# Performance work log

Hardware: AMD Instinct MI355X
Metric: run time of the kernel (lower is better)

The kernel has to match this reference:

```python
import jax, jax.numpy as jnp
import numpy as np

N = 50000          # nodes
E = 1_600_000      # edges (avg degree 32, radius graph capped at 64 nbrs)
F_X = 32           # node feature dim
F_E = 8            # edge attr dim
RADIUS = 8.0       # radius used to normalize pair distance
EPS = 1e-5         # LayerNorm eps (torch default)


def _glorot(key, shape):
    fan_in = shape[0]
    return (jax.random.normal(key, shape, dtype=jnp.float32) / np.sqrt(fan_in)).astype(jnp.float32)


def setup_inputs() -> dict:
    key = jax.random.key(0)
    ks = jax.random.split(key, 16)
    x = jax.random.normal(ks[0], (N, F_X), dtype=jnp.float32)
    pos = jax.random.normal(ks[1], (N, 3), dtype=jnp.float32) * 10.0
    normal = jax.random.normal(ks[2], (N, 3), dtype=jnp.float32)
    normal = normal / jnp.linalg.norm(normal, axis=1, keepdims=True)
    edge_attr = jax.random.normal(ks[3], (E, F_E), dtype=jnp.float32)
    edge_index = jax.random.randint(ks[4], (2, E), 0, N, dtype=jnp.int64)
    d_in = F_X + 7 + F_E  # 47
    return {
        "x": x, "pos": pos, "normal": normal, "edge_attr": edge_attr,
        "edge_index": edge_index,
        # local MLP: [47 -> 64 -> 128], each block Linear->ReLU->LayerNorm
        "W1": _glorot(ks[5], (d_in, 64)), "b1": jnp.zeros((64,), jnp.float32),
        "g1": jnp.ones((64,), jnp.float32), "be1": jnp.zeros((64,), jnp.float32),
        "W2": _glorot(ks[6], (64, 128)), "b2": jnp.zeros((128,), jnp.float32),
        "g2": jnp.ones((128,), jnp.float32), "be2": jnp.zeros((128,), jnp.float32),
        # global MLP: [128 -> 256]
        "Wg": _glorot(ks[7], (128, 256)), "bg": jnp.zeros((256,), jnp.float32),
        "gg": jnp.ones((256,), jnp.float32), "beg": jnp.zeros((256,), jnp.float32),
    }


def _layernorm(h, g, b):
    mu = jnp.mean(h, axis=-1, keepdims=True)
    var = jnp.mean(jnp.square(h - mu), axis=-1, keepdims=True)
    return (h - mu) * jax.lax.rsqrt(var + EPS) * g + b


def _mlp_block(h, W, b, g, be):
    # Linear -> ReLU -> LayerNorm (Dropout inactive in eval mode)
    return _layernorm(jax.nn.relu(h @ W + b), g, be)


def _angle(v1, v2):
    cross = jnp.cross(v1, v2)
    return jnp.arctan2(jnp.linalg.norm(cross, axis=1), jnp.sum(v1 * v2, axis=1))


def reference(x, pos, normal, edge_attr, edge_index,
              W1, b1, g1, be1, W2, b2, g2, be2, Wg, bg, gg, beg):
    src = edge_index[0]  # j (source)
    dst = edge_index[1]  # i (target)
    pos_i, pos_j = pos[dst], pos[src]
    n_i, n_j = normal[dst], normal[src]
    pseudo = pos_j - pos_i                       # [E,3]
    a1 = _angle(n_i, pseudo)
    a2 = _angle(n_j, pseudo)
    a3 = _angle(n_i, n_j)
    ppf = jnp.stack([
        jnp.linalg.norm(pseudo, axis=1) / RADIUS,
        jnp.sin(a1), jnp.cos(a1),
        jnp.sin(a2), jnp.cos(a2),
        jnp.sin(a3), jnp.cos(a3),
    ], axis=1)                                   # [E,7]
    msg = jnp.concatenate([x[src], ppf, edge_attr], axis=1)  # [E,47]
    msg = _mlp_block(msg, W1, b1, g1, be1)       # [E,64]
    msg = _mlp_block(msg, W2, b2, g2, be2)       # [E,128]
    agg = jax.ops.segment_max(msg, dst, num_segments=N)      # [N,128]
    agg = jnp.where(jnp.isfinite(agg), agg, 0.0)  # nodes with no in-edges -> 0
    out = _mlp_block(agg, Wg, bg, gg, beg)       # [N,256]
    return out
```

## Files before the change

### kernel.cpp

```cpp
#include <hip/hip_runtime.h>
#include <hip/hip_bf16.h>
#include <math.h>


#define LN_EPS 1e-5f
#define EPB 128
#define SM 72
#define SP 130
#define AS 132

typedef __attribute__((ext_vector_type(8))) short bf16x8;
typedef __attribute__((ext_vector_type(4))) float floatx4;
typedef __attribute__((ext_vector_type(4))) short s4v;

__device__ __forceinline__ unsigned ord(float f) {
    int i = __float_as_int(f);
    return (i >= 0) ? ((unsigned)i | 0x80000000u) : ~((unsigned)i);
}
__device__ __forceinline__ float unord(unsigned u) {
    int i = (u & 0x80000000u) ? (int)(u & 0x7fffffffu) : ~(int)u;
    return __int_as_float(i);
}
__device__ __forceinline__ unsigned short f2b(float f) {
    unsigned u = __float_as_uint(f);
    return (unsigned short)((u + 0x7FFFu + ((u >> 16) & 1u)) >> 16);
}
__device__ __forceinline__ float b2f(unsigned short h) {
    return __uint_as_float((unsigned)h << 16);
}

__global__ void hist_kernel(const int* __restrict__ ei, unsigned* __restrict__ deg, int E) {
    int e = blockIdx.x * 256 + threadIdx.x;
    if (e < E) atomicAdd(&deg[ei[E + e]], 1u);
}

__global__ void scan1(const unsigned* __restrict__ deg, unsigned* __restrict__ part, int N) {
    __shared__ unsigned s[256];
    int i = blockIdx.x * 256 + threadIdx.x;
    s[threadIdx.x] = (i < N) ? deg[i] : 0u;
    __syncthreads();
    for (int st = 128; st > 0; st >>= 1) {
        if (threadIdx.x < st) s[threadIdx.x] += s[threadIdx.x + st];
        __syncthreads();
    }
    if (threadIdx.x == 0) part[blockIdx.x] = s[0];
}

__global__ void scan2(unsigned* __restrict__ part, int nb) {
    __shared__ unsigned s[256];
    int t = threadIdx.x;
    unsigned v = (t < nb) ? part[t] : 0u;
    s[t] = v;
    __syncthreads();
    for (int st = 1; st < 256; st <<= 1) {
        unsigned add = (t >= st) ? s[t - st] : 0u;
        __syncthreads();
        s[t] += add;
        __syncthreads();
    }
    if (t < nb) part[t] = s[t] - v;
}

__global__ void scan3(const unsigned* __restrict__ deg, const unsigned* __restrict__ part,
                      unsigned* __restrict__ off, int N) {
    __shared__ unsigned s[256];
    int i = blockIdx.x * 256 + threadIdx.x, t = threadIdx.x;
    unsigned v = (i < N) ? deg[i] : 0u;
    s[t] = v;
    __syncthreads();
    for (int st = 1; st < 256; st <<= 1) {
        unsigned add = (t >= st) ? s[t - st] : 0u;
        __syncthreads();
        s[t] += add;
        __syncthreads();
    }
    if (i < N) off[i] = part[blockIdx.x] + s[t] - v;
}

__global__ void scatter_kernel(const int* __restrict__ ei, unsigned* __restrict__ cursor,
                               unsigned* __restrict__ perm, int* __restrict__ dsts, int E) {
    int e = blockIdx.x * 256 + threadIdx.x;
    if (e >= E) return;
    int d = ei[E + e];
    unsigned pos = atomicAdd(&cursor[d], 1u);
    perm[pos] = (unsigned)e;
    dsts[pos] = d;
}

__global__ void wprep_kernel(const float* __restrict__ W1, const float* __restrict__ W2,
                             const float* __restrict__ Wg,
                             unsigned short* __restrict__ W1p, unsigned short* __restrict__ W2p,
                             unsigned short* __restrict__ Wgp)
{
    int t = threadIdx.x;
    for (int fl = t; fl < 8 * 64; fl += 256) {
        int fi = fl >> 6, l = fl & 63;
        int s = fi >> 2, nt = fi & 3;
        int n = nt * 16 + (l & 15);
        int kb = s * 32 + ((l >> 4) << 3);
        #pragma unroll
        for (int j = 0; j < 8; ++j) {
            int k = kb + j;
            W1p[fl * 8 + j] = f2b((k < 47) ? W1[k * 64 + n] : 0.f);
        }
    }
    for (int fl = t; fl < 16 * 64; fl += 256) {
        int fi = fl >> 6, l = fl & 63;
        int s = fi >> 3, nt = fi & 7;
        int n = nt * 16 + (l & 15);
        int kb = s * 32 + ((l >> 4) << 3);
        #pragma unroll
        for (int j = 0; j < 8; ++j)
            W2p[fl * 8 + j] = f2b(W2[(kb + j) * 128 + n]);
    }
    for (int fl = t; fl < 64 * 64; fl += 256) {
        int fi = fl >> 6, l = fl & 63;
        int s = fi >> 4, nt = fi & 15;
        int n = nt * 16 + (l & 15);
        int kb = s * 32 + ((l >> 4) << 3);
        #pragma unroll
        for (int j = 0; j < 8; ++j)
            Wgp[fl * 8 + j] = f2b(Wg[(size_t)(kb + j) * 256 + n]);
    }
}

__global__ __launch_bounds__(256, 2)
void edge_kernel(const float* __restrict__ x,
                 const float* __restrict__ pos,
                 const float* __restrict__ nrm,
                 const float* __restrict__ ea,
                 const int* __restrict__ ei,
                 const unsigned* __restrict__ perm,
                 const int* __restrict__ dsts,
                 const unsigned short* __restrict__ W1p, const float* __restrict__ b1,
                 const float* __restrict__ g1, const float* __restrict__ be1,
                 const unsigned short* __restrict__ W2p, const float* __restrict__ b2,
                 const float* __restrict__ g2, const float* __restrict__ be2,
                 unsigned* __restrict__ agg, int E)
{
    __shared__ unsigned short hbuf[EPB * SM];
    __shared__ unsigned short st[128 * SP];
    __shared__ int dloc[EPB];
    __shared__ short rstart[EPB], rend[EPB];
    __shared__ unsigned long long wmask[2];
    __shared__ int dprev_s, dnext_s;

    const int tid  = threadIdx.x;
    const int lane = tid & 63;
    const int half = tid >> 7;
    const int el   = tid & 127;
    const int base = blockIdx.x * EPB;
    const int p    = base + el;
    const bool valid = p < E;
    const int nvalid = (E - base < EPB) ? (E - base) : EPB;

    int dst = 0, src = 0, e = 0;
    if (valid) {
        e   = (int)perm[p];
        dst = dsts[p];
        src = ei[e];
    }
    if (half == 0) dloc[el] = valid ? dst : -1;
    if (tid == 0) {
        dprev_s = (blockIdx.x == 0) ? -1 : dsts[(size_t)base - 1];
        dnext_s = (base + EPB < E) ? dsts[base + EPB] : -1;
    }

    if (valid) {
        unsigned short* row = &hbuf[el * SM];
        if (half == 0) {
            const float4* xp = (const float4*)(x + (size_t)src * 32);
            #pragma unroll
            for (int q = 0; q < 4; ++q) {
                float4 v = xp[q];
                s4v h = { (short)f2b(v.x), (short)f2b(v.y), (short)f2b(v.z), (short)f2b(v.w) };
                *(s4v*)&row[4 * q] = h;
            }
            float pix = pos[3*dst+0], piy = pos[3*dst+1], piz = pos[3*dst+2];
            float pjx = pos[3*src+0], pjy = pos[3*src+1], pjz = pos[3*src+2];
            float dx = pjx - pix, dy = pjy - piy, dz = pjz - piz;
            float nix = nrm[3*dst+0], niy = nrm[3*dst+1], niz = nrm[3*dst+2];
            float njx = nrm[3*src+0], njy = nrm[3*src+1], njz = nrm[3*src+2];
            row[32] = f2b(sqrtf(dx*dx + dy*dy + dz*dz) * 0.125f);
            float cx, cy, cz, c2, d, den, inv, sn, cs;
            cx = niy*dz - niz*dy; cy = niz*dx - nix*dz; cz = nix*dy - niy*dx;
            c2 = cx*cx + cy*cy + cz*cz;  d = nix*dx + niy*dy + niz*dz;
            den = c2 + d*d;
            if (den > 0.f) { inv = rsqrtf(den); sn = sqrtf(c2)*inv; cs = d*inv; }
            else           { sn = 0.f; cs = 1.f; }
            row[33] = f2b(sn); row[34] = f2b(cs);
            cx = njy*dz - njz*dy; cy = njz*dx - njx*dz; cz = njx*dy - njy*dx;
            c2 = cx*cx + cy*cy + cz*cz;  d = njx*dx + njy*dy + njz*dz;
            den = c2 + d*d;
            if (den > 0.f) { inv = rsqrtf(den); sn = sqrtf(c2)*inv; cs = d*inv; }
            else           { sn = 0.f; cs = 1.f; }
            row[35] = f2b(sn); row[36] = f2b(cs);
            cx = niy*njz - niz*njy; cy = niz*njx - nix*njz; cz = nix*njy - niy*njx;
            c2 = cx*cx + cy*cy + cz*cz;  d = nix*njx + niy*njy + niz*njz;
            den = c2 + d*d;
            if (den > 0.f) { inv = rsqrtf(den); sn = sqrtf(c2)*inv; cs = d*inv; }
            else           { sn = 0.f; cs = 1.f; }
            row[37] = f2b(sn); row[38] = f2b(cs);
        } else {
            const float4* xp = (const float4*)(x + (size_t)src * 32) + 4;
            #pragma unroll
            for (int q = 0; q < 4; ++q) {
                float4 v = xp[q];
                s4v h = { (short)f2b(v.x), (short)f2b(v.y), (short)f2b(v.z), (short)f2b(v.w) };
                *(s4v*)&row[16 + 4 * q] = h;
            }
            const float4* ep = (const float4*)(ea + (size_t)e * 8);
            float4 a0 = ep[0], a1 = ep[1];
            row[39] = f2b(a0.x); row[40] = f2b(a0.y);
            row[41] = f2b(a0.z); row[42] = f2b(a0.w);
            row[43] = f2b(a1.x); row[44] = f2b(a1.y);
            row[45] = f2b(a1.z); row[46] = f2b(a1.w);
            row[47] = 0;
            s4v z = {0, 0, 0, 0};
            *(s4v*)&row[48] = z; *(s4v*)&row[52] = z;
            *(s4v*)&row[56] = z; *(s4v*)&row[60] = z;
        }
    }
    __syncthreads();

    bool is_start = false, is_end = false;
    if (tid < 128) {
        int dt = dloc[tid];
        bool isv = tid < nvalid;
        is_start = isv && (tid == 0 || dloc[tid - 1] != dt);
        is_end   = isv && (tid == nvalid - 1 || dloc[tid + 1] != dt);
    }
    {
        unsigned long long mb = __ballot(is_start);
        if ((tid >> 6) < 2 && lane == 0) wmask[tid >> 6] = mb;
    }
    __syncthreads();
    int nr;
    {
        unsigned long long m0 = wmask[0], m1 = wmask[1];
        nr = __popcll(m0) + __popcll(m1);
        if (tid < 128) {
            int widr = tid >> 6;
            int rid = (widr ? __popcll(m0) : 0)
                    + __popcll((widr ? m1 : m0) & ((1ull << lane) - 1ull));
            if (is_start) rstart[rid] = (short)tid;
            if (is_end)   rend[is_start ? rid : rid - 1] = (short)tid;
        }
    }

    const int wid  = __builtin_amdgcn_readfirstlane(tid >> 6);
    const int quad = lane >> 4, col = lane & 15;
    const int mb0  = wid * 32;

    {
        bf16x8 w1f[8];
        const bf16x8* W1v = (const bf16x8*)W1p;
        #pragma unroll
        for (int i = 0; i < 8; ++i) w1f[i] = W1v[i * 64 + lane];
        float b1v[4], g1v[4], e1v[4];
        #pragma unroll
        for (int nt = 0; nt < 4; ++nt) {
            b1v[nt] = b1[nt*16 + col]; g1v[nt] = g1[nt*16 + col]; e1v[nt] = be1[nt*16 + col];
        }
        #pragma unroll
        for (int t = 0; t < 2; ++t) {
            const int mb = mb0 + t * 16;
            floatx4 acc[4] = {{0,0,0,0},{0,0,0,0},{0,0,0,0},{0,0,0,0}};
            #pragma unroll
            for (int s = 0; s < 2; ++s) {
                const unsigned short* ap = &hbuf[(mb + col) * SM + s*32 + quad*8];
                union { s4v h[2]; bf16x8 v; } u;
                u.h[0] = *(const s4v*)ap; u.h[1] = *(const s4v*)(ap + 4);
                #pragma unroll
                for (int nt = 0; nt < 4; ++nt)
                    acc[nt] = __builtin_amdgcn_mfma_f32_16x16x32_bf16(u.v, w1f[s*4+nt], acc[nt], 0, 0, 0);
            }
            float ps[4] = {0,0,0,0}, p2[4] = {0,0,0,0};
            #pragma unroll
            for (int nt = 0; nt < 4; ++nt)
                #pragma unroll
                for (int r = 0; r < 4; ++r) {
                    float v = fmaxf(acc[nt][r] + b1v[nt], 0.f);
                    acc[nt][r] = v; ps[r] += v; p2[r] += v * v;
                }
            #pragma unroll
            for (int r = 0; r < 4; ++r) {
                #pragma unroll
                for (int m = 1; m < 16; m <<= 1) {
                    ps[r] += __shfl_xor(ps[r], m);
                    p2[r] += __shfl_xor(p2[r], m);
                }
            }
            float mu[4], rs[4];
            #pragma unroll
            for (int r = 0; r < 4; ++r) {
                mu[r] = ps[r] * (1.f/64.f);
                float var = fmaxf(p2[r] * (1.f/64.f) - mu[r]*mu[r], 0.f);
                rs[r] = rsqrtf(var + LN_EPS);
            }
            #pragma unroll
            for (int nt = 0; nt < 4; ++nt)
                #pragma unroll
                for (int r = 0; r < 4; ++r) {
                    float hn = (acc[nt][r] - mu[r]) * rs[r] * g1v[nt] + e1v[nt];
                    hbuf[(mb + quad*4 + r) * SM + nt*16 + col] = f2b(hn);
                }
        }
    }
    {
        bf16x8 w2f[16];
        const bf16x8* W2v = (const bf16x8*)W2p;
        #pragma unroll
        for (int i = 0; i < 16; ++i) w2f[i] = W2v[i * 64 + lane];
        float b2v[8], g2v[8], e2v[8];
        #pragma unroll
        for (int nt = 0; nt < 8; ++nt) {
            b2v[nt] = b2[nt*16 + col]; g2v[nt] = g2[nt*16 + col]; e2v[nt] = be2[nt*16 + col];
        }
        #pragma unroll
        for (int t = 0; t < 2; ++t) {
            const int mb = mb0 + t * 16;
            floatx4 acc[8] = {{0,0,0,0},{0,0,0,0},{0,0,0,0},{0,0,0,0},
                              {0,0,0,0},{0,0,0,0},{0,0,0,0},{0,0,0,0}};
            #pragma unroll
            for (int s = 0; s < 2; ++s) {
                const unsigned short* ap = &hbuf[(mb + col) * SM + s*32 + quad*8];
                union { s4v h[2]; bf16x8 v; } u;
                u.h[0] = *(const s4v*)ap; u.h[1] = *(const s4v*)(ap + 4);
                #pragma unroll
                for (int nt = 0; nt < 8; ++nt)
                    acc[nt] = __builtin_amdgcn_mfma_f32_16x16x32_bf16(u.v, w2f[s*8+nt], acc[nt], 0, 0, 0);
            }
            float ps[4] = {0,0,0,0}, p2[4] = {0,0,0,0};
            #pragma unroll
            for (int nt = 0; nt < 8; ++nt)
                #pragma unroll
                for (int r = 0; r < 4; ++r) {
                    float v = fmaxf(acc[nt][r] + b2v[nt], 0.f);
                    acc[nt][r] = v; ps[r] += v; p2[r] += v * v;
                }
            #pragma unroll
            for (int r = 0; r < 4; ++r) {
                #pragma unroll
                for (int m = 1; m < 16; m <<= 1) {
                    ps[r] += __shfl_xor(ps[r], m);
                    p2[r] += __shfl_xor(p2[r], m);
                }
            }
            float mu[4], rs[4];
            #pragma unroll
            for (int r = 0; r < 4; ++r) {
                mu[r] = ps[r] * (1.f/128.f);
                float var = fmaxf(p2[r] * (1.f/128.f) - mu[r]*mu[r], 0.f);
                rs[r] = rsqrtf(var + LN_EPS);
            }
            #pragma unroll
            for (int nt = 0; nt < 8; ++nt)
                #pragma unroll
                for (int r = 0; r < 4; ++r) {
                    float hn = (acc[nt][r] - mu[r]) * rs[r] * g2v[nt] + e2v[nt];
                    st[(nt*16 + col) * SP + (mb + quad*4 + r)] = f2b(hn);
                }
        }
    }
    __syncthreads();

    {
        const int grp = tid >> 7;
        const int f   = tid & 127;
        const unsigned short* fr = &st[f * SP];
        for (int r = grp; r < nr; r += 2) {
            int s0 = rstart[r], en = rend[r];
            int d  = dloc[s0];
            float v0 = -1e30f, v1 = -1e30f, v2 = -1e30f, v3 = -1e30f;
            int c = s0;
            for (; c + 3 <= en; c += 4) {
                v0 = fmaxf(v0, b2f(fr[c]));
                v1 = fmaxf(v1, b2f(fr[c + 1]));
                v2 = fmaxf(v2, b2f(fr[c + 2]));
                v3 = fmaxf(v3, b2f(fr[c + 3]));
            }
            for (; c <= en; ++c) v0 = fmaxf(v0, b2f(fr[c]));
            float val = fmaxf(fmaxf(v0, v1), fmaxf(v2, v3));
            bool contPrev = (s0 == 0) && (dprev_s == d);
            bool contNext = (en == nvalid - 1) && (dnext_s == d);
            unsigned enc = ord(val);
            unsigned* ap = agg + (size_t)d * 128 + f;
            if (contPrev || contNext) atomicMax(ap, enc);
            else                      *ap = enc;
        }
    }
}

__global__ __launch_bounds__(256, 2)
void node_kernel(const unsigned* __restrict__ agg,
                 const unsigned short* __restrict__ Wgp, const float* __restrict__ bg,
                 const float* __restrict__ gg, const float* __restrict__ beg,
                 float* __restrict__ out, int N)
{
    __shared__ unsigned short a_bf[64 * AS];
    const int tid  = threadIdx.x;
    const int base = blockIdx.x * 64;
    const size_t total = (size_t)N * 128;

    #pragma unroll
    for (int i = 0; i < 32; ++i) {
        int idx = tid + i * 256;
        int nl = idx >> 7, k = idx & 127;
        size_t g = (size_t)base * 128 + idx;
        unsigned u = (g < total) ? agg[g] : 0u;
        a_bf[nl * AS + k] = (u == 0u) ? (unsigned short)0 : f2b(unord(u));
    }
    __syncthreads();

    const int lane = tid & 63;
    const int wid  = __builtin_amdgcn_readfirstlane(tid >> 6);
    const int quad = lane >> 4, col = lane & 15;
    const int m0   = wid * 16;

    bf16x8 af[4];
    #pragma unroll
    for (int s = 0; s < 4; ++s) {
        const unsigned short* ap = &a_bf[(m0 + col) * AS + s*32 + quad*8];
        union { s4v h[2]; bf16x8 v; } u;
        u.h[0] = *(const s4v*)ap; u.h[1] = *(const s4v*)(ap + 4);
        af[s] = u.v;
    }

    float accv[16][4];
    float ps[4] = {0,0,0,0}, p2[4] = {0,0,0,0};
    const bf16x8* Wv = (const bf16x8*)Wgp;
    #pragma unroll
    for (int nt = 0; nt < 16; ++nt) {
        floatx4 acc = {0, 0, 0, 0};
        #pragma unroll
        for (int s = 0; s < 4; ++s)
            acc = __builtin_amdgcn_mfma_f32_16x16x32_bf16(af[s], Wv[(s*16 + nt)*64 + lane], acc, 0, 0, 0);
        float b = bg[nt*16 + col];
        #pragma unroll
        for (int r = 0; r < 4; ++r) {
            float v = fmaxf(acc[r] + b, 0.f);
            accv[nt][r] = v; ps[r] += v; p2[r] += v * v;
        }
    }
    #pragma unroll
    for (int r = 0; r < 4; ++r) {
        #pragma unroll
        for (int m = 1; m < 16; m <<= 1) {
            ps[r] += __shfl_xor(ps[r], m);
            p2[r] += __shfl_xor(p2[r], m);
        }
    }
    float mu[4], rs[4];
    #pragma unroll
    for (int r = 0; r < 4; ++r) {
        mu[r] = ps[r] * (1.f/256.f);
        float var = fmaxf(p2[r] * (1.f/256.f) - mu[r]*mu[r], 0.f);
        rs[r] = rsqrtf(var + LN_EPS);
    }
    #pragma unroll
    for (int nt = 0; nt < 16; ++nt) {
        float g = gg[nt*16 + col], be = beg[nt*16 + col];
        #pragma unroll
        for (int r = 0; r < 4; ++r) {
            int node = base + m0 + quad*4 + r;
            if (node < N)
                out[(size_t)node * 256 + nt*16 + col] = (accv[nt][r] - mu[r]) * rs[r] * g + be;
        }
    }
}

extern "C" void kernel_launch(void* const* d_in, const int* in_sizes, int n_in,
                              void* d_out, int out_size, void* d_ws, size_t ws_size,
                              hipStream_t stream) {
    const float* x         = (const float*)d_in[0];
    const float* pos       = (const float*)d_in[1];
    const float* nrm       = (const float*)d_in[2];
    const float* edge_attr = (const float*)d_in[3];
    const int*   ei        = (const int*)d_in[4];
    const float* W1  = (const float*)d_in[5];
    const float* b1  = (const float*)d_in[6];
    const float* g1  = (const float*)d_in[7];
    const float* be1 = (const float*)d_in[8];
    const float* W2  = (const float*)d_in[9];
    const float* b2  = (const float*)d_in[10];
    const float* g2  = (const float*)d_in[11];
    const float* be2 = (const float*)d_in[12];
    const float* Wg  = (const float*)d_in[13];
    const float* bg  = (const float*)d_in[14];
    const float* gg  = (const float*)d_in[15];
    const float* beg = (const float*)d_in[16];

    const int E = in_sizes[3] / 8;
    const int N = in_sizes[0] / 32;

    char* ws = (char*)d_ws;
    unsigned* agg  = (unsigned*)ws;                   ws += (size_t)N * 128 * 4;
    unsigned* deg  = (unsigned*)ws;                   ws += (size_t)N * 4;
    unsigned* off  = (unsigned*)ws;                   ws += (size_t)N * 4;
    unsigned* part = (unsigned*)ws;                   ws += 256 * 4;
    unsigned* perm = (unsigned*)ws;                   ws += (size_t)E * 4;
    int*      dsts = (int*)ws;                        ws += (size_t)E * 4;
    unsigned short* W1p = (unsigned short*)ws;        ws += 8 * 64 * 8 * 2;
    unsigned short* W2p = (unsigned short*)ws;        ws += 16 * 64 * 8 * 2;
    unsigned short* Wgp = (unsigned short*)ws;        ws += 64 * 64 * 8 * 2;

    hipMemsetAsync(agg, 0, (size_t)N * 128 * 4, stream);
    hipMemsetAsync(deg, 0, (size_t)N * 4, stream);

    hipLaunchKernelGGL(wprep_kernel, dim3(1), dim3(256), 0, stream, W1, W2, Wg, W1p, W2p, Wgp);

    const int nbN = (N + 255) / 256;
    hipLaunchKernelGGL(hist_kernel, dim3((E + 255) / 256), dim3(256), 0, stream, ei, deg, E);
    hipLaunchKernelGGL(scan1, dim3(nbN), dim3(256), 0, stream, deg, part, N);
    hipLaunchKernelGGL(scan2, dim3(1), dim3(256), 0, stream, part, nbN);
    hipLaunchKernelGGL(scan3, dim3(nbN), dim3(256), 0, stream, deg, part, off, N);
    hipLaunchKernelGGL(scatter_kernel, dim3((E + 255) / 256), dim3(256), 0, stream,
                       ei, off, perm, dsts, E);

    hipLaunchKernelGGL(edge_kernel, dim3((E + EPB - 1) / EPB), dim3(256), 0, stream,
                       x, pos, nrm, edge_attr, ei, perm, dsts,
                       W1p, b1, g1, be1, W2p, b2, g2, be2, agg, E);

    hipLaunchKernelGGL(node_kernel, dim3((N + 63) / 64), dim3(256), 0, stream,
                       agg, Wgp, bg, gg, beg, (float*)d_out, N);
}
```

Before: 652.8 us.

## Vectorize CSR build, drop dsts array, pack bf16 conversions, widen segment-max reads

The histogram and scatter kernels now handle four edges per thread using int4 loads. The separate dsts array is removed, so the edge kernel recovers each destination through ei[E+perm[p]], which is an extra dependent gather. Bf16 conversion and LDS stores are packed two values at a time, and the per-feature segment max reads 32-bit words. Weight prep is spread over 16 blocks instead of one. Together these cut launch and write traffic in preprocessing at the cost of an indirect load in the main kernel.

```diff
diff --git a/kernel.cpp b/kernel.cpp
--- a/kernel.cpp
+++ b/kernel.cpp
@@ -28,10 +28,26 @@
 __device__ __forceinline__ float b2f(unsigned short h) {
     return __uint_as_float((unsigned)h << 16);
 }
+__device__ __forceinline__ unsigned f2b2(float lo, float hi) {
+    union { __hip_bfloat162 h2; unsigned u; } c;
+    c.h2 = __float22bfloat162_rn(make_float2(lo, hi));
+    return c.u;
+}
+__device__ __forceinline__ float b2f_lo(unsigned w) { return __uint_as_float(w << 16); }
+__device__ __forceinline__ float b2f_hi(unsigned w) { return __uint_as_float(w & 0xFFFF0000u); }
 
 __global__ void hist_kernel(const int* __restrict__ ei, unsigned* __restrict__ deg, int E) {
-    int e = blockIdx.x * 256 + threadIdx.x;
-    if (e < E) atomicAdd(&deg[ei[E + e]], 1u);
+    int b4 = (blockIdx.x * 256 + threadIdx.x) * 4;
+    if (b4 + 3 < E) {
+        int4 d4 = *(const int4*)(ei + E + b4);
+        atomicAdd(&deg[d4.x], 1u);
+        atomicAdd(&deg[d4.y], 1u);
+        atomicAdd(&deg[d4.z], 1u);
+        atomicAdd(&deg[d4.w], 1u);
+    } else {
+        for (int i = 0; i < 4; ++i)
+            if (b4 + i < E) atomicAdd(&deg[ei[E + b4 + i]], 1u);
+    }
 }
 
 __global__ void scan1(const unsigned* __restrict__ deg, unsigned* __restrict__ part, int N) {
@@ -78,13 +94,21 @@
 }
 
 __global__ void scatter_kernel(const int* __restrict__ ei, unsigned* __restrict__ cursor,
-                               unsigned* __restrict__ perm, int* __restrict__ dsts, int E) {
-    int e = blockIdx.x * 256 + threadIdx.x;
-    if (e >= E) return;
-    int d = ei[E + e];
-    unsigned pos = atomicAdd(&cursor[d], 1u);
-    perm[pos] = (unsigned)e;
-    dsts[pos] = d;
+                               unsigned* __restrict__ perm, int E) {
+    int b4 = (blockIdx.x * 256 + threadIdx.x) * 4;
+    if (b4 + 3 < E) {
+        int4 d4 = *(const int4*)(ei + E + b4);
+        perm[atomicAdd(&cursor[d4.x], 1u)] = (unsigned)(b4 + 0);
+        perm[atomicAdd(&cursor[d4.y], 1u)] = (unsigned)(b4 + 1);
+        perm[atomicAdd(&cursor[d4.z], 1u)] = (unsigned)(b4 + 2);
+        perm[atomicAdd(&cursor[d4.w], 1u)] = (unsigned)(b4 + 3);
+    } else {
+        for (int i = 0; i < 4; ++i)
+            if (b4 + i < E) {
+                int d = ei[E + b4 + i];
+                perm[atomicAdd(&cursor[d], 1u)] = (unsigned)(b4 + i);
+            }
+    }
 }
 
 __global__ void wprep_kernel(const float* __restrict__ W1, const float* __restrict__ W2,
@@ -92,8 +116,9 @@
                              unsigned short* __restrict__ W1p, unsigned short* __restrict__ W2p,
                              unsigned short* __restrict__ Wgp)
 {
-    int t = threadIdx.x;
-    for (int fl = t; fl < 8 * 64; fl += 256) {
+    int gt = blockIdx.x * 256 + threadIdx.x;
+    int gs = gridDim.x * 256;
+    for (int fl = gt; fl < 8 * 64; fl += gs) {
         int fi = fl >> 6, l = fl & 63;
         int s = fi >> 2, nt = fi & 3;
         int n = nt * 16 + (l & 15);
@@ -104,7 +129,7 @@
             W1p[fl * 8 + j] = f2b((k < 47) ? W1[k * 64 + n] : 0.f);
         }
     }
-    for (int fl = t; fl < 16 * 64; fl += 256) {
+    for (int fl = gt; fl < 16 * 64; fl += gs) {
         int fi = fl >> 6, l = fl & 63;
         int s = fi >> 3, nt = fi & 7;
         int n = nt * 16 + (l & 15);
@@ -113,7 +138,7 @@
         for (int j = 0; j < 8; ++j)
             W2p[fl * 8 + j] = f2b(W2[(kb + j) * 128 + n]);
     }
-    for (int fl = t; fl < 64 * 64; fl += 256) {
+    for (int fl = gt; fl < 64 * 64; fl += gs) {
         int fi = fl >> 6, l = fl & 63;
         int s = fi >> 4, nt = fi & 15;
         int n = nt * 16 + (l & 15);
@@ -131,7 +156,6 @@
                  const float* __restrict__ ea,
                  const int* __restrict__ ei,
                  const unsigned* __restrict__ perm,
-                 const int* __restrict__ dsts,
                  const unsigned short* __restrict__ W1p, const float* __restrict__ b1,
                  const float* __restrict__ g1, const float* __restrict__ be1,
                  const unsigned short* __restrict__ W2p, const float* __restrict__ b2,
@@ -157,14 +181,14 @@
     int dst = 0, src = 0, e = 0;
     if (valid) {
         e   = (int)perm[p];
-        dst = dsts[p];
         src = ei[e];
+        dst = ei[E + e];
     }
     if (half == 0) dloc[el] = valid ? dst : -1;
-    if (tid == 0) {
-        dprev_s = (blockIdx.x == 0) ? -1 : dsts[(size_t)base - 1];
-        dnext_s = (base + EPB < E) ? dsts[base + EPB] : -1;
-    }
+    if (tid == 0)
+        dprev_s = (blockIdx.x == 0) ? -1 : ei[E + (int)perm[(size_t)base - 1]];
+    if (tid == 1)
+        dnext_s = (base + EPB < E) ? ei[E + (int)perm[base + EPB]] : -1;
 
     if (valid) {
         unsigned short* row = &hbuf[el * SM];
@@ -173,8 +197,7 @@
             #pragma unroll
             for (int q = 0; q < 4; ++q) {
                 float4 v = xp[q];
-                s4v h = { (short)f2b(v.x), (short)f2b(v.y), (short)f2b(v.z), (short)f2b(v.w) };
-                *(s4v*)&row[4 * q] = h;
+                *(uint2*)&row[4 * q] = make_uint2(f2b2(v.x, v.y), f2b2(v.z, v.w));
             }
             float pix = pos[3*dst+0], piy = pos[3*dst+1], piz = pos[3*dst+2];
             float pjx = pos[3*src+0], pjy = pos[3*src+1], pjz = pos[3*src+2];
@@ -206,19 +229,16 @@
             #pragma unroll
             for (int q = 0; q < 4; ++q) {
                 float4 v = xp[q];
-                s4v h = { (short)f2b(v.x), (short)f2b(v.y), (short)f2b(v.z), (short)f2b(v.w) };
-                *(s4v*)&row[16 + 4 * q] = h;
+                *(uint2*)&row[16 + 4 * q] = make_uint2(f2b2(v.x, v.y), f2b2(v.z, v.w));
             }
             const float4* ep = (const float4*)(ea + (size_t)e * 8);
             float4 a0 = ep[0], a1 = ep[1];
-            row[39] = f2b(a0.x); row[40] = f2b(a0.y);
-            row[41] = f2b(a0.z); row[42] = f2b(a0.w);
-            row[43] = f2b(a1.x); row[44] = f2b(a1.y);
-            row[45] = f2b(a1.z); row[46] = f2b(a1.w);
-            row[47] = 0;
-            s4v z = {0, 0, 0, 0};
-            *(s4v*)&row[48] = z; *(s4v*)&row[52] = z;
-            *(s4v*)&row[56] = z; *(s4v*)&row[60] = z;
+            row[39] = f2b(a0.x);
+            *(uint2*)&row[40] = make_uint2(f2b2(a0.y, a0.z), f2b2(a0.w, a1.x));
+            *(uint2*)&row[44] = make_uint2(f2b2(a1.y, a1.z), f2b2(a1.w, 0.f));
+            uint2 z = make_uint2(0u, 0u);
+            *(uint2*)&row[48] = z; *(uint2*)&row[52] = z;
+            *(uint2*)&row[56] = z; *(uint2*)&row[60] = z;
         }
     }
     __syncthreads();
@@ -299,12 +319,16 @@
                 rs[r] = rsqrtf(var + LN_EPS);
             }
             #pragma unroll
-            for (int nt = 0; nt < 4; ++nt)
-                #pragma unroll
-                for (int r = 0; r < 4; ++r) {
-                    float hn = (acc[nt][r] - mu[r]) * rs[r] * g1v[nt] + e1v[nt];
-                    hbuf[(mb + quad*4 + r) * SM + nt*16 + col] = f2b(hn);
+            for (int nt = 0; nt < 4; ++nt) {
+                #pragma unroll
+                for (int r = 0; r < 4; r += 2) {
+                    float h0 = (acc[nt][r]   - mu[r])   * rs[r]   * g1v[nt] + e1v[nt];
+                    float h1 = (acc[nt][r+1] - mu[r+1]) * rs[r+1] * g1v[nt] + e1v[nt];
+                    unsigned pk = f2b2(h0, h1);
+                    hbuf[(mb + quad*4 + r)   * SM + nt*16 + col] = (unsigned short)pk;
+                    hbuf[(mb + quad*4 + r+1) * SM + nt*16 + col] = (unsigned short)(pk >> 16);
                 }
+            }
         }
     }
     {
@@ -355,12 +379,15 @@
                 rs[r] = rsqrtf(var + LN_EPS);
             }
             #pragma unroll
-            for (int nt = 0; nt < 8; ++nt)
-                #pragma unroll
-                for (int r = 0; r < 4; ++r) {
-                    float hn = (acc[nt][r] - mu[r]) * rs[r] * g2v[nt] + e2v[nt];
-                    st[(nt*16 + col) * SP + (mb + quad*4 + r)] = f2b(hn);
-                }
+            for (int nt = 0; nt < 8; ++nt) {
+                float h0 = (acc[nt][0] - mu[0]) * rs[0] * g2v[nt] + e2v[nt];
+                float h1 = (acc[nt][1] - mu[1]) * rs[1] * g2v[nt] + e2v[nt];
+                float h2 = (acc[nt][2] - mu[2]) * rs[2] * g2v[nt] + e2v[nt];
+                float h3 = (acc[nt][3] - mu[3]) * rs[3] * g2v[nt] + e2v[nt];
+                unsigned* d32 = (unsigned*)&st[(nt*16 + col) * SP + mb + quad*4];
+                d32[0] = f2b2(h0, h1);
+                d32[1] = f2b2(h2, h3);
+            }
         }
     }
     __syncthreads();
@@ -369,19 +396,25 @@
         const int grp = tid >> 7;
         const int f   = tid & 127;
         const unsigned short* fr = &st[f * SP];
+        const unsigned* fp = (const unsigned*)fr;
         for (int r = grp; r < nr; r += 2) {
             int s0 = rstart[r], en = rend[r];
             int d  = dloc[s0];
-            float v0 = -1e30f, v1 = -1e30f, v2 = -1e30f, v3 = -1e30f;
+            float v0 = -1e30f, v1 = -1e30f;
             int c = s0;
+            if (c & 1) { v0 = fmaxf(v0, b2f(fr[c])); ++c; }
             for (; c + 3 <= en; c += 4) {
-                v0 = fmaxf(v0, b2f(fr[c]));
-                v1 = fmaxf(v1, b2f(fr[c + 1]));
-                v2 = fmaxf(v2, b2f(fr[c + 2]));
-                v3 = fmaxf(v3, b2f(fr[c + 3]));
-            }
-            for (; c <= en; ++c) v0 = fmaxf(v0, b2f(fr[c]));
-            float val = fmaxf(fmaxf(v0, v1), fmaxf(v2, v3));
+                unsigned wa = fp[c >> 1], wb = fp[(c >> 1) + 1];
+                v0 = fmaxf(v0, fmaxf(b2f_lo(wa), b2f_hi(wa)));
+                v1 = fmaxf(v1, fmaxf(b2f_lo(wb), b2f_hi(wb)));
+            }
+            if (c + 1 <= en) {
+                unsigned wa = fp[c >> 1];
+                v0 = fmaxf(v0, fmaxf(b2f_lo(wa), b2f_hi(wa)));
+                c += 2;
+            }
+            if (c <= en) v0 = fmaxf(v0, b2f(fr[c]));
+            float val = fmaxf(v0, v1);
             bool contPrev = (s0 == 0) && (dprev_s == d);
             bool contNext = (en == nvalid - 1) && (dnext_s == d);
             unsigned enc = ord(val);
@@ -500,7 +533,6 @@
     unsigned* off  = (unsigned*)ws;                   ws += (size_t)N * 4;
     unsigned* part = (unsigned*)ws;                   ws += 256 * 4;
     unsigned* perm = (unsigned*)ws;                   ws += (size_t)E * 4;
-    int*      dsts = (int*)ws;                        ws += (size_t)E * 4;
     unsigned short* W1p = (unsigned short*)ws;        ws += 8 * 64 * 8 * 2;
     unsigned short* W2p = (unsigned short*)ws;        ws += 16 * 64 * 8 * 2;
     unsigned short* Wgp = (unsigned short*)ws;        ws += 64 * 64 * 8 * 2;
@@ -508,18 +540,18 @@
     hipMemsetAsync(agg, 0, (size_t)N * 128 * 4, stream);
     hipMemsetAsync(deg, 0, (size_t)N * 4, stream);
 
-    hipLaunchKernelGGL(wprep_kernel, dim3(1), dim3(256), 0, stream, W1, W2, Wg, W1p, W2p, Wgp);
+    hipLaunchKernelGGL(wprep_kernel, dim3(16), dim3(256), 0, stream, W1, W2, Wg, W1p, W2p, Wgp);
 
     const int nbN = (N + 255) / 256;
-    hipLaunchKernelGGL(hist_kernel, dim3((E + 255) / 256), dim3(256), 0, stream, ei, deg, E);
+    const int nbE4 = (E + 1023) / 1024;
+    hipLaunchKernelGGL(hist_kernel, dim3(nbE4), dim3(256), 0, stream, ei, deg, E);
     hipLaunchKernelGGL(scan1, dim3(nbN), dim3(256), 0, stream, deg, part, N);
     hipLaunchKernelGGL(scan2, dim3(1), dim3(256), 0, stream, part, nbN);
     hipLaunchKernelGGL(scan3, dim3(nbN), dim3(256), 0, stream, deg, part, off, N);
-    hipLaunchKernelGGL(scatter_kernel, dim3((E + 255) / 256), dim3(256), 0, stream,
-                       ei, off, perm, dsts, E);
+    hipLaunchKernelGGL(scatter_kernel, dim3(nbE4), dim3(256), 0, stream, ei, off, perm, E);
 
     hipLaunchKernelGGL(edge_kernel, dim3((E + EPB - 1) / EPB), dim3(256), 0, stream,
-                       x, pos, nrm, edge_attr, ei, perm, dsts,
+                       x, pos, nrm, edge_attr, ei, perm,
                        W1p, b1, g1, be1, W2p, b2, g2, be2, agg, E);
 
     hipLaunchKernelGGL(node_kernel, dim3((N + 63) / 64), dim3(256), 0, stream,
```

New measurement: 607.7 us. 1.07x faster.
